# Performance work log

Hardware: AMD Instinct MI355X
Metric: run time of the kernel (lower is better)

Reference implementation:

```python
import jax, jax.numpy as jnp
import numpy as np

B, T, C, H = 4, 2048, 1024, 16
D = C // H  # head dim = 64


def setup_inputs() -> dict:
    key = jax.random.key(0)
    ks = jax.random.split(key, 5)
    s = 0.02
    return {
        "x": jax.random.normal(ks[0], (B, T, C), dtype=jnp.float32),
        "W_attn": jax.random.normal(ks[1], (C, 3 * C), dtype=jnp.float32) * s,
        "b_attn": jnp.zeros((3 * C,), dtype=jnp.float32),
        "W_proj": jax.random.normal(ks[2], (C, C), dtype=jnp.float32) * s,
        "b_proj": jnp.zeros((C,), dtype=jnp.float32),
    }


def reference(x, W_attn, b_attn, W_proj, b_proj):
    # qkv projection: [B,T,3C]
    qkv = x @ W_attn + b_attn
    q, k, v = jnp.split(qkv, 3, axis=-1)
    # [B,T,C] -> [B,H,T,D]
    def heads(t):
        return t.reshape(B, T, H, D).transpose(0, 2, 1, 3)
    q, k, v = heads(q), heads(k), heads(v)
    # scaled scores with causal mask, materialized [B,H,T,T] as in original
    att = jnp.einsum('bhqd,bhkd->bhqk', q, k) * (1.0 / np.sqrt(D))
    causal = jnp.tril(jnp.ones((T, T), dtype=bool))
    att = jnp.where(causal[None, None], att, -jnp.inf)
    att = jax.nn.softmax(att, axis=-1)
    y = jnp.einsum('bhqk,bhkd->bhqd', att, v)  # [B,H,T,D]
    y = y.transpose(0, 2, 1, 3).reshape(B, T, C)
    y = y @ W_proj + b_proj
    # original also returns present=(k,v); it is a pure pass-through cache
    return y
```

## Files before the change

### kernel.cpp

```cpp
#include <hip/hip_runtime.h>


typedef unsigned short u16;
typedef unsigned int u32;
typedef __attribute__((ext_vector_type(8))) unsigned short u16x8;
typedef __attribute__((ext_vector_type(4))) unsigned short u16x4;
typedef __attribute__((ext_vector_type(8))) short short8;
typedef __attribute__((ext_vector_type(4))) float f32x4;

__device__ inline u16 f2bf(float f) {
  unsigned u = __float_as_uint(f);
  u = (u + 0x7FFF + ((u >> 16) & 1)) >> 16;
  return (u16)u;
}

__device__ inline f32x4 mfma16(short8 a, short8 b, f32x4 c) {
  return __builtin_amdgcn_mfma_f32_16x16x32_bf16(a, b, c, 0, 0, 0);
}

__device__ inline void tw_tile(const float* __restrict__ in,
                               u16* __restrict__ outT, int R, int Cc,
                               int c0, int r0, int tid, u16 (*t)[65]) {
  int a = tid & 63, w = tid >> 6;
#pragma unroll
  for (int j = 0; j < 16; ++j) {
    int r = w + j * 4;
    t[r][a] = f2bf(in[(size_t)(r0 + r) * Cc + c0 + a]);
  }
  __syncthreads();
#pragma unroll
  for (int j = 0; j < 16; ++j) {
    int c = w + j * 4;
    outT[(size_t)(c0 + c) * R + r0 + a] = t[a][c];
  }
}

__global__ __launch_bounds__(256) void k_prep(const float* __restrict__ x,
                                              u16* __restrict__ xb,
                                              const float* __restrict__ Wa,
                                              u16* __restrict__ wta,
                                              const float* __restrict__ Wp,
                                              u16* __restrict__ wtp) {
  __shared__ u16 t[64][65];
  const int id = blockIdx.x, tid = threadIdx.x;
  if (id < 8192) {
    int i = (id * 256 + tid) * 4;
    float4 v = *(const float4*)(x + i);
    u16x4 o = {f2bf(v.x), f2bf(v.y), f2bf(v.z), f2bf(v.w)};
    *(u16x4*)(xb + i) = o;
  } else if (id < 8960) {
    int q = id - 8192;
    tw_tile(Wa, wta, 1024, 3072, (q % 48) * 64, (q / 48) * 64, tid, t);
  } else {
    int q = id - 8960;
    tw_tile(Wp, wtp, 1024, 1024, (q % 16) * 64, (q / 16) * 64, tid, t);
  }
}

template <int OUTBF, int QSCALE, int VT>
__global__ __launch_bounds__(256) void gemm_bt(const u16* __restrict__ A,
                                               const u16* __restrict__ Bt,
                                               const float* __restrict__ bias,
                                               u16* __restrict__ outb,
                                               float* __restrict__ outf,
                                               u16* __restrict__ vtout,
                                               int M, int N, int K) {
  __shared__ u16 As[128 * 64];
  __shared__ u16 Bs[128 * 64];
  const int nx = gridDim.x, ny = gridDim.y;
  int id0 = blockIdx.x + blockIdx.y * nx;
  int nwg = nx * ny;
  int q8 = nwg >> 3, x8 = id0 & 7, c8 = id0 >> 3;
  int id = x8 * q8 + c8;
  int gs = 8 * ny, grp = id / gs, rem = id % gs;
  const int m0 = (grp * 8 + (rem & 7)) * 128, n0 = (rem >> 3) * 128;

  const int tid = threadIdx.x, wave = tid >> 6, lane = tid & 63;
  const int quad = lane >> 4, l16 = lane & 15;
  const int wm = (wave & 1) * 64, wn = (wave >> 1) * 64;
  const int lrow = lane >> 3;
  const int lch = lane & 7;
  const int slot = lch ^ lrow;
  const u16* sA[4];
  const u16* sB[4];
  int offA[4], offB[4];
#pragma unroll
  for (int j = 0; j < 4; ++j) {
    int r = wave * 32 + j * 8;
    sA[j] = A + (size_t)(m0 + r + lrow) * K + lch * 8;
    sB[j] = Bt + (size_t)(n0 + r + lrow) * K + lch * 8;
    offA[j] = (r + lrow) * 64 + slot * 8;
    offB[j] = offA[j];
  }
  u16x8 ra[4], rb[4];
#pragma unroll
  for (int j = 0; j < 4; ++j) {
    ra[j] = *(const u16x8*)(sA[j]);
    rb[j] = *(const u16x8*)(sB[j]);
  }
  f32x4 acc[4][4] = {};
  for (int kt = 0; kt < K; kt += 64) {
    __syncthreads();
#pragma unroll
    for (int j = 0; j < 4; ++j) {
      *(u16x8*)&As[offA[j]] = ra[j];
      *(u16x8*)&Bs[offB[j]] = rb[j];
    }
    __syncthreads();
    if (kt + 64 < K) {
#pragma unroll
      for (int j = 0; j < 4; ++j) {
        ra[j] = *(const u16x8*)(sA[j] + kt + 64);
        rb[j] = *(const u16x8*)(sB[j] + kt + 64);
      }
    }
    const int sl = l16 & 7;
#pragma unroll
    for (int ks = 0; ks < 2; ++ks) {
      short8 af[4], bf[4];
#pragma unroll
      for (int mt = 0; mt < 4; ++mt)
        af[mt] = *(const short8*)(As + (wm + mt * 16 + l16) * 64 +
                                  ((ks * 4 + quad) ^ sl) * 8);
#pragma unroll
      for (int nt = 0; nt < 4; ++nt)
        bf[nt] = *(const short8*)(Bs + (wn + nt * 16 + l16) * 64 +
                                  ((ks * 4 + quad) ^ sl) * 8);
#pragma unroll
      for (int mt = 0; mt < 4; ++mt)
#pragma unroll
        for (int nt = 0; nt < 4; ++nt)
          acc[mt][nt] = mfma16(af[mt], bf[nt], acc[mt][nt]);
    }
  }
#pragma unroll
  for (int nt = 0; nt < 4; ++nt) {
    int col = n0 + wn + nt * 16 + l16;
    float bv = bias[col];
    if (VT && col >= 2048) {
      const int hd = col - 2048;
#pragma unroll
      for (int mt = 0; mt < 4; ++mt) {
        int rowb = m0 + wm + mt * 16 + quad * 4;
        int bb = rowb >> 11, t0 = rowb & 2047;
        u16x4 pk;
#pragma unroll
        for (int r = 0; r < 4; ++r) pk[r] = f2bf(acc[mt][nt][r] + bv);
        *(u16x4*)(vtout + ((size_t)(bb << 10) + hd) * 2048 + t0) = pk;
      }
    } else {
#pragma unroll
      for (int mt = 0; mt < 4; ++mt) {
        int rowb = m0 + wm + mt * 16 + quad * 4;
#pragma unroll
        for (int r = 0; r < 4; ++r) {
          float v = acc[mt][nt][r] + bv;
          if (QSCALE && col < 1024) v *= 0.18033688f;
          if (OUTBF)
            outb[(size_t)(rowb + r) * N + col] = f2bf(v);
          else
            outf[(size_t)(rowb + r) * N + col] = v;
        }
      }
    }
  }
}

#define ATP 72
__global__ __launch_bounds__(256) void attn(const u16* __restrict__ qkv,
                                            const u16* __restrict__ vt,
                                            u16* __restrict__ y) {
  __shared__ u16 shm[384 * ATP];
  u16* Qs = shm;
  const int p = blockIdx.x, h = blockIdx.y, b = blockIdx.z;
  const int tid = threadIdx.x, wave = tid >> 6, lane = tid & 63;
  const int quad = lane >> 4, l16 = lane & 15;
  const u16* Qg = qkv + (size_t)b * 2048 * 3072 + h * 64;
  const u16* Kg = Qg + 1024;
  const u16* Vtg = vt + (size_t)(b * 16 + h) * 64 * 2048;
  const int srow0 = tid >> 3, scol0 = (tid & 7) * 8;
  u16* Pw0 = Qs + (wave * 16) * ATP;
  u16* Pw1 = Qs + (64 + wave * 16) * ATP;
  short8 ones_f;
#pragma unroll
  for (int j = 0; j < 8; ++j) ones_f[j] = 0x3F80;

  for (int half = 0; half < 2; ++half) {
    const int qb = half ? (15 - p) : p;
    const int q0 = qb * 128;
    const int nkt = 2 * qb + 2;
    auto kadr0 = [&](int t) { return Kg + (size_t)(64 * t + srow0) * 3072 + scol0; };
    auto vadr0 = [&](int t) { return Vtg + (size_t)srow0 * 2048 + 64 * t + scol0; };
    u16x8 qr0 = *(const u16x8*)(Qg + (size_t)(q0 + srow0) * 3072 + scol0);
    u16x8 qr1 = *(const u16x8*)(Qg + (size_t)(q0 + srow0 + 32) * 3072 + scol0);
    u16x8 qr2 = *(const u16x8*)(Qg + (size_t)(q0 + srow0 + 64) * 3072 + scol0);
    u16x8 qr3 = *(const u16x8*)(Qg + (size_t)(q0 + srow0 + 96) * 3072 + scol0);
    u16x8 kreg0 = *(const u16x8*)(kadr0(0));
    u16x8 kreg1 = *(const u16x8*)(kadr0(0) + 32 * 3072);
    u16x8 vreg0 = *(const u16x8*)(vadr0(0));
    u16x8 vreg1 = *(const u16x8*)(vadr0(0) + 32 * 2048);
    __syncthreads();
    *(u16x8*)&Qs[(size_t)srow0 * ATP + scol0] = qr0;
    *(u16x8*)&Qs[(size_t)(srow0 + 32) * ATP + scol0] = qr1;
    *(u16x8*)&Qs[(size_t)(srow0 + 64) * ATP + scol0] = qr2;
    *(u16x8*)&Qs[(size_t)(srow0 + 96) * ATP + scol0] = qr3;
    {
      u16* Kb = shm + 128 * ATP;
      u16* Vb = Kb + 64 * ATP;
      *(u16x8*)&Kb[(size_t)srow0 * ATP + scol0] = kreg0;
      *(u16x8*)&Kb[(size_t)(srow0 + 32) * ATP + scol0] = kreg1;
      *(u16x8*)&Vb[(size_t)srow0 * ATP + scol0] = vreg0;
      *(u16x8*)&Vb[(size_t)(srow0 + 32) * ATP + scol0] = vreg1;
    }
    if (nkt > 1) {
      kreg0 = *(const u16x8*)(kadr0(1));
      kreg1 = *(const u16x8*)(kadr0(1) + 32 * 3072);
      vreg0 = *(const u16x8*)(vadr0(1));
      vreg1 = *(const u16x8*)(vadr0(1) + 32 * 2048);
    }
    __syncthreads();
    short8 qf0a = *(const short8*)&Qs[(wave * 16 + l16) * ATP + quad * 8];
    short8 qf1a = *(const short8*)&Qs[(wave * 16 + l16) * ATP + 32 + quad * 8];
    short8 qf0b = *(const short8*)&Qs[(64 + wave * 16 + l16) * ATP + quad * 8];
    short8 qf1b = *(const short8*)&Qs[(64 + wave * 16 + l16) * ATP + 32 + quad * 8];

    f32x4 lacc0 = {}, lacc1 = {};
    f32x4 o0[4] = {}, o1[4] = {};

    auto tile = [&](int kt, int g0mode, bool g1mask) {
      if (kt > 0) __syncthreads();
      if (kt + 1 < nkt) {
        u16* Kw = shm + (128 + 128 * ((kt + 1) & 1)) * ATP;
        u16* Vw = Kw + 64 * ATP;
        *(u16x8*)&Kw[(size_t)srow0 * ATP + scol0] = kreg0;
        *(u16x8*)&Kw[(size_t)(srow0 + 32) * ATP + scol0] = kreg1;
        *(u16x8*)&Vw[(size_t)srow0 * ATP + scol0] = vreg0;
        *(u16x8*)&Vw[(size_t)(srow0 + 32) * ATP + scol0] = vreg1;
      }
      if (kt + 2 < nkt) {
        kreg0 = *(const u16x8*)(kadr0(kt + 2));
        kreg1 = *(const u16x8*)(kadr0(kt + 2) + 32 * 3072);
        vreg0 = *(const u16x8*)(vadr0(kt + 2));
        vreg1 = *(const u16x8*)(vadr0(kt + 2) + 32 * 2048);
      }
      const u16* Ks = shm + (128 + 128 * (kt & 1)) * ATP;
      const u16* Vs = Ks + 64 * ATP;

      f32x4 s0[4] = {}, s1[4] = {};
#pragma unroll
      for (int mt = 0; mt < 4; ++mt) {
        short8 kf0 = *(const short8*)&Ks[(mt * 16 + l16) * ATP + quad * 8];
        short8 kf1 = *(const short8*)&Ks[(mt * 16 + l16) * ATP + 32 + quad * 8];
        if (g0mode < 2) {
          s0[mt] = mfma16(kf0, qf0a, s0[mt]);
          s0[mt] = mfma16(kf1, qf1a, s0[mt]);
        }
        s1[mt] = mfma16(kf0, qf0b, s1[mt]);
        s1[mt] = mfma16(kf1, qf1b, s1[mt]);
      }

      if (g0mode < 2) {
        const int qrow = q0 + wave * 16 + l16;
#pragma unroll
        for (int mt = 0; mt < 4; ++mt) {
          float pe[4];
#pragma unroll
          for (int r = 0; r < 4; ++r) {
            float pv = __builtin_amdgcn_exp2f(s0[mt][r]);
            if (g0mode == 1) {
              int kcol = kt * 64 + mt * 16 + quad * 4 + r;
              if (kcol > qrow) pv = 0.f;
            }
            pe[r] = pv;
          }
          u32 lo = __builtin_amdgcn_perm(__float_as_uint(pe[1]),
                                         __float_as_uint(pe[0]), 0x07060302u);
          u32 hi = __builtin_amdgcn_perm(__float_as_uint(pe[3]),
                                         __float_as_uint(pe[2]), 0x07060302u);
          uint2 pk = {lo, hi};
          *(uint2*)&Pw0[l16 * ATP + mt * 16 + quad * 4] = pk;
        }
      }
      {
        const int qrow = q0 + 64 + wave * 16 + l16;
#pragma unroll
        for (int mt = 0; mt < 4; ++mt) {
          float pe[4];
#pragma unroll
          for (int r = 0; r < 4; ++r) {
            float pv = __builtin_amdgcn_exp2f(s1[mt][r]);
            if (g1mask) {
              int kcol = kt * 64 + mt * 16 + quad * 4 + r;
              if (kcol > qrow) pv = 0.f;
            }
            pe[r] = pv;
          }
          u32 lo = __builtin_amdgcn_perm(__float_as_uint(pe[1]),
                                         __float_as_uint(pe[0]), 0x07060302u);
          u32 hi = __builtin_amdgcn_perm(__float_as_uint(pe[3]),
                                         __float_as_uint(pe[2]), 0x07060302u);
          uint2 pk = {lo, hi};
          *(uint2*)&Pw1[l16 * ATP + mt * 16 + quad * 4] = pk;
        }
      }

#pragma unroll
      for (int ks = 0; ks < 2; ++ks) {
        short8 pf0, pf1;
        if (g0mode < 2) {
          pf0 = *(const short8*)&Pw0[l16 * ATP + ks * 32 + quad * 8];
          lacc0 = mfma16(pf0, ones_f, lacc0);
        }
        pf1 = *(const short8*)&Pw1[l16 * ATP + ks * 32 + quad * 8];
        lacc1 = mfma16(pf1, ones_f, lacc1);
#pragma unroll
        for (int dt = 0; dt < 4; ++dt) {
          short8 vf = *(const short8*)&Vs[(dt * 16 + l16) * ATP + ks * 32 + quad * 8];
          if (g0mode < 2) o0[dt] = mfma16(pf0, vf, o0[dt]);
          o1[dt] = mfma16(pf1, vf, o1[dt]);
        }
      }
    };

    for (int kt = 0; kt < nkt - 2; ++kt) tile(kt, 0, false);
    tile(nkt - 2, 1, false);
    tile(nkt - 1, 2, true);

    size_t rb0 = (size_t)b * 2048 + q0 + wave * 16 + quad * 4;
#pragma unroll
    for (int r = 0; r < 4; ++r) {
      float inv = 1.f / lacc0[r];
#pragma unroll
      for (int dt = 0; dt < 4; ++dt)
        y[(rb0 + r) * 1024 + h * 64 + dt * 16 + l16] = f2bf(o0[dt][r] * inv);
    }
    size_t rb1 = rb0 + 64;
#pragma unroll
    for (int r = 0; r < 4; ++r) {
      float inv = 1.f / lacc1[r];
#pragma unroll
      for (int dt = 0; dt < 4; ++dt)
        y[(rb1 + r) * 1024 + h * 64 + dt * 16 + l16] = f2bf(o1[dt][r] * inv);
    }
  }
}

extern "C" void kernel_launch(void* const* d_in, const int* in_sizes, int n_in,
                              void* d_out, int out_size, void* d_ws, size_t ws_size,
                              hipStream_t stream) {
  const float* x = (const float*)d_in[0];
  const float* W_attn = (const float*)d_in[1];
  const float* b_attn = (const float*)d_in[2];
  const float* W_proj = (const float*)d_in[3];
  const float* b_proj = (const float*)d_in[4];
  float* out = (float*)d_out;
  char* ws = (char*)d_ws;
  u16* xb  = (u16*)(ws);
  u16* wta = (u16*)(ws + 16777216);
  u16* wtp = (u16*)(ws + 23068672);
  u16* qkv = (u16*)(ws + 25165824);
  u16* vt  = (u16*)(ws + 75497472);
  u16* y   = (u16*)(ws + 92274688);

  k_prep<<<dim3(9216), 256, 0, stream>>>(x, xb, W_attn, wta, W_proj, wtp);
  gemm_bt<1, 1, 1><<<dim3(64, 24), 256, 0, stream>>>(xb, wta, b_attn, qkv, nullptr, vt, 8192, 3072, 1024);
  attn<<<dim3(8, 16, 4), 256, 0, stream>>>(qkv, vt, y);
  gemm_bt<0, 0, 0><<<dim3(64, 8), 256, 0, stream>>>(y, wtp, b_proj, nullptr, out, nullptr, 8192, 1024, 1024);
}
```

Baseline: 237.0 us.

## Double-buffer LDS tiles in GEMM to drop one barrier per k-step

Switches the bf16 GEMM's shared-memory A/B tiles to double buffering. Each iteration writes the next tile into the alternate buffer and issues global loads two tiles ahead, so only one __syncthreads per k-step is needed instead of two. The aim is to overlap LDS stores and global loads with MFMA compute and cut barrier stalls. In exchange, LDS use doubles to 64KB per block, which may lower occupancy.

```diff
diff --git a/kernel.cpp b/kernel.cpp
--- a/kernel.cpp
+++ b/kernel.cpp
@@ -65,8 +65,8 @@
                                                float* __restrict__ outf,
                                                u16* __restrict__ vtout,
                                                int M, int N, int K) {
-  __shared__ u16 As[128 * 64];
-  __shared__ u16 Bs[128 * 64];
+  __shared__ u16 As[2 * 128 * 64];
+  __shared__ u16 Bs[2 * 128 * 64];
   const int nx = gridDim.x, ny = gridDim.y;
   int id0 = blockIdx.x + blockIdx.y * nx;
   int nwg = nx * ny;
@@ -92,26 +92,42 @@
     offA[j] = (r + lrow) * 64 + slot * 8;
     offB[j] = offA[j];
   }
+  const int nt = K >> 6;
   u16x8 ra[4], rb[4];
 #pragma unroll
   for (int j = 0; j < 4; ++j) {
     ra[j] = *(const u16x8*)(sA[j]);
     rb[j] = *(const u16x8*)(sB[j]);
   }
+#pragma unroll
+  for (int j = 0; j < 4; ++j) {
+    *(u16x8*)&As[offA[j]] = ra[j];
+    *(u16x8*)&Bs[offB[j]] = rb[j];
+  }
+  if (nt > 1) {
+#pragma unroll
+    for (int j = 0; j < 4; ++j) {
+      ra[j] = *(const u16x8*)(sA[j] + 64);
+      rb[j] = *(const u16x8*)(sB[j] + 64);
+    }
+  }
+  __syncthreads();
   f32x4 acc[4][4] = {};
-  for (int kt = 0; kt < K; kt += 64) {
-    __syncthreads();
-#pragma unroll
-    for (int j = 0; j < 4; ++j) {
-      *(u16x8*)&As[offA[j]] = ra[j];
-      *(u16x8*)&Bs[offB[j]] = rb[j];
-    }
-    __syncthreads();
-    if (kt + 64 < K) {
+  for (int t = 0; t < nt; ++t) {
+    const int cur = (t & 1) * 8192;
+    if (t + 1 < nt) {
+      const int nxt = 8192 - cur;
 #pragma unroll
       for (int j = 0; j < 4; ++j) {
-        ra[j] = *(const u16x8*)(sA[j] + kt + 64);
-        rb[j] = *(const u16x8*)(sB[j] + kt + 64);
+        *(u16x8*)&As[nxt + offA[j]] = ra[j];
+        *(u16x8*)&Bs[nxt + offB[j]] = rb[j];
+      }
+    }
+    if (t + 2 < nt) {
+#pragma unroll
+      for (int j = 0; j < 4; ++j) {
+        ra[j] = *(const u16x8*)(sA[j] + (t + 2) * 64);
+        rb[j] = *(const u16x8*)(sB[j] + (t + 2) * 64);
       }
     }
     const int sl = l16 & 7;
@@ -120,22 +136,23 @@
       short8 af[4], bf[4];
 #pragma unroll
       for (int mt = 0; mt < 4; ++mt)
-        af[mt] = *(const short8*)(As + (wm + mt * 16 + l16) * 64 +
+        af[mt] = *(const short8*)(As + cur + (wm + mt * 16 + l16) * 64 +
                                   ((ks * 4 + quad) ^ sl) * 8);
 #pragma unroll
-      for (int nt = 0; nt < 4; ++nt)
-        bf[nt] = *(const short8*)(Bs + (wn + nt * 16 + l16) * 64 +
-                                  ((ks * 4 + quad) ^ sl) * 8);
+      for (int nt2 = 0; nt2 < 4; ++nt2)
+        bf[nt2] = *(const short8*)(Bs + cur + (wn + nt2 * 16 + l16) * 64 +
+                                   ((ks * 4 + quad) ^ sl) * 8);
 #pragma unroll
       for (int mt = 0; mt < 4; ++mt)
 #pragma unroll
-        for (int nt = 0; nt < 4; ++nt)
-          acc[mt][nt] = mfma16(af[mt], bf[nt], acc[mt][nt]);
-    }
-  }
-#pragma unroll
-  for (int nt = 0; nt < 4; ++nt) {
-    int col = n0 + wn + nt * 16 + l16;
+        for (int nt2 = 0; nt2 < 4; ++nt2)
+          acc[mt][nt2] = mfma16(af[mt], bf[nt2], acc[mt][nt2]);
+    }
+    if (t + 1 < nt) __syncthreads();
+  }
+#pragma unroll
+  for (int nt2 = 0; nt2 < 4; ++nt2) {
+    int col = n0 + wn + nt2 * 16 + l16;
     float bv = bias[col];
     if (VT && col >= 2048) {
       const int hd = col - 2048;
@@ -145,7 +162,7 @@
         int bb = rowb >> 11, t0 = rowb & 2047;
         u16x4 pk;
 #pragma unroll
-        for (int r = 0; r < 4; ++r) pk[r] = f2bf(acc[mt][nt][r] + bv);
+        for (int r = 0; r < 4; ++r) pk[r] = f2bf(acc[mt][nt2][r] + bv);
         *(u16x4*)(vtout + ((size_t)(bb << 10) + hd) * 2048 + t0) = pk;
       }
     } else {
@@ -154,7 +171,7 @@
         int rowb = m0 + wm + mt * 16 + quad * 4;
 #pragma unroll
         for (int r = 0; r < 4; ++r) {
-          float v = acc[mt][nt][r] + bv;
+          float v = acc[mt][nt2][r] + bv;
           if (QSCALE && col < 1024) v *= 0.18033688f;
           if (OUTBF)
             outb[(size_t)(rowb + r) * N + col] = f2bf(v);
```

After: 238.8 us. Within noise of the previous version (+0.8%).
